# Performance work log

Measured on AMD Instinct MI355X. Metric: run time of the kernel, lower is better.

Reference implementation:

```python
import jax, jax.numpy as jnp
import numpy as np

S_IN = 14; KERNEL = 3; STRIDE = 1; C_IN = 32; C_OUT = 32; BATCH = 4; ROUTINGS = 3
EPS = 1e-7

def _child_parent_map(size_in, kernel, stride):
    # Same construction as BaseCaps._generate_voting_map: for each output position,
    # the flattened indices of its kernel window in the size_in x size_in grid.
    rows = []
    for row in range(0, size_in - kernel + 1, stride):
        for col in range(0, size_in - kernel + 1, stride):
            w = []
            for kr in range(kernel):
                start = (row + kr) * size_in + col
                w.extend(range(start, start + kernel))
            rows.append(w)
    return np.array(rows, dtype=np.int32)  # [size_out^2, kernel^2]

def setup_inputs() -> dict:
    key = jax.random.key(0)
    ks = jax.random.split(key, 5)
    in_act = jax.random.uniform(ks[0], (BATCH, S_IN, S_IN, C_IN, 1), jnp.float32)
    in_pose = jax.random.normal(ks[1], (BATCH, S_IN, S_IN, C_IN, 4, 4), jnp.float32)
    W = jax.random.normal(ks[2], (KERNEL * KERNEL * C_IN, C_OUT, 4, 4), jnp.float32) * 0.1
    beta_v = jax.random.normal(ks[3], (C_OUT,), jnp.float32)
    beta_a = jax.random.normal(ks[4], (C_OUT,), jnp.float32)
    cpm = jnp.asarray(_child_parent_map(S_IN, KERNEL, STRIDE))
    return {"in_act": in_act, "in_pose": in_pose, "transformation_weights": W,
            "beta_a": beta_a, "beta_v": beta_v, "child_parent_map": cpm}

def em_routing(act, votes, beta_a, beta_v, routings):
    # act: [B,P,K,1,1]  votes: [B,P,K,C,16]
    B, P, K, C, D = votes.shape
    rr = jnp.full((B, P, K, C, 1), 1.0 / C, votes.dtype)
    it_min, it_max = 1.0, max(1.0, min(float(routings), 3.0))
    out_a = out_mu = None
    for i in range(routings):
        inv_temp = it_min + (it_max - it_min) * (i / max(1.0, routings - 1.0))
        # --- M-step ---
        rp = rr * act                                        # [B,P,K,C,1]
        rs = rp.sum(axis=2, keepdims=True) + EPS             # [B,P,1,C,1]
        mu = (rp * votes).sum(axis=2, keepdims=True) / rs    # [B,P,1,C,D]
        var = (rp * (votes - mu) ** 2).sum(axis=2, keepdims=True) / rs + EPS
        cost = (beta_v[:, None] + 0.5 * jnp.log(var)) * rs   # [B,P,1,C,D]
        out_a = jax.nn.sigmoid(inv_temp * (beta_a[:, None] - cost.sum(-1, keepdims=True)))
        # --- E-step ---
        if i < routings - 1:
            log_p = -0.5 * jnp.sum(jnp.log(2.0 * jnp.pi * var) + (votes - mu) ** 2 / var,
                                   axis=-1, keepdims=True)   # [B,P,K,C,1]
            rr = jax.nn.softmax(jnp.log(out_a + EPS) + log_p, axis=3)
        out_mu = mu
    return out_a[:, :, 0, :, 0], out_mu[:, :, 0]  # [B,P,C], [B,P,C,D]

def reference(in_act, in_pose, transformation_weights, beta_a, beta_v, child_parent_map):
    B, S, _, Cin, _ = in_act.shape
    P, Kw = child_parent_map.shape           # [out_spatial^2, kernel^2]
    Sout = int(round(P ** 0.5))
    C = transformation_weights.shape[1]
    act = in_act.reshape(B, S * S, Cin)
    pose = in_pose.reshape(B, S * S, Cin, 4, 4)
    # gather kernel windows of child capsules per output position
    act_g = act[:, child_parent_map].reshape(B, P, Kw * Cin)             # [B,P,K]
    pose_g = pose[:, child_parent_map].reshape(B, P, Kw * Cin, 4, 4)     # [B,P,K,4,4]
    # votes = child_pose @ W, per (child k, parent capsule c)
    votes = jnp.einsum('bpkij,kcjl->bpkcil', pose_g, transformation_weights)
    votes = votes.reshape(B, P, Kw * Cin, C, 16)
    out_a, out_mu = em_routing(act_g[..., None, None], votes, beta_a, beta_v, ROUTINGS)
    out_act = out_a.reshape(B, Sout, Sout, C, 1)
    out_pose = out_mu.reshape(B, Sout, Sout, C, 4, 4)
    return out_act, out_pose
```

## Files before the change

kernel.cpp:

```cpp
#include <hip/hip_runtime.h>
#include <math.h>

#define NB 4
#define NP 144
#define KW 9
#define CIN 32
#define NC 32
#define NK 288
#define ND 16
#define NDH 8
#define EPSI 1e-7f
#define NT 256
#define KPT 36
#define NRED 2


typedef float v2f __attribute__((ext_vector_type(2)));

__device__ __forceinline__ v2f mkv2(float a, float b) { v2f r; r[0] = a; r[1] = b; return r; }

template<int CTRL>
__device__ __forceinline__ float dppf(float x) {
    return __int_as_float(__builtin_amdgcn_update_dpp(
        0, __float_as_int(x), CTRL, 0xF, 0xF, true));
}
__device__ __forceinline__ float swz16(float x) {
    return __int_as_float(__builtin_amdgcn_ds_swizzle(__float_as_int(x), 0x401F));
}
__device__ __forceinline__ float red16_max(float x) {
    x = fmaxf(x, dppf<0xB1>(x));
    x = fmaxf(x, dppf<0x4E>(x));
    x = fmaxf(x, dppf<0x141>(x));
    x = fmaxf(x, dppf<0x140>(x));
    return x;
}
__device__ __forceinline__ float red16_sum(float x) {
    x += dppf<0xB1>(x);
    x += dppf<0x4E>(x);
    x += dppf<0x141>(x);
    x += dppf<0x140>(x);
    return x;
}

__device__ __forceinline__ int sw4(int c, int j) { return j ^ ((c >> 1) & 3); }

__device__ __forceinline__ void load16(const float* src, float* dst) {
    const float4* s4 = (const float4*)src;
    *(float4*)&dst[0]  = s4[0];
    *(float4*)&dst[4]  = s4[1];
    *(float4*)&dst[8]  = s4[2];
    *(float4*)&dst[12] = s4[3];
}
__device__ __forceinline__ void load16v(const float* src, v2f* dst) {
    const float4* s4 = (const float4*)src;
    #pragma unroll
    for (int q = 0; q < 4; ++q) {
        const float4 tq = s4[q];
        dst[q*2+0] = mkv2(tq.x, tq.y);
        dst[q*2+1] = mkv2(tq.z, tq.w);
    }
}

__device__ __forceinline__ void vote44v(const float* pr, const v2f* wr2, v2f* v2) {
    #pragma unroll
    for (int i = 0; i < 4; ++i) {
        const v2f p0 = mkv2(pr[i*4+0], pr[i*4+0]);
        const v2f p1 = mkv2(pr[i*4+1], pr[i*4+1]);
        const v2f p2 = mkv2(pr[i*4+2], pr[i*4+2]);
        const v2f p3 = mkv2(pr[i*4+3], pr[i*4+3]);
        #pragma unroll
        for (int p = 0; p < 2; ++p) {
            v2f acc = p0 * wr2[0*2+p];
            acc += p1 * wr2[1*2+p];
            acc += p2 * wr2[2*2+p];
            acc += p3 * wr2[3*2+p];
            v2[i*2+p] = acc;
        }
    }
}

__device__ __forceinline__ void reduce_finalize(
    float r0, v2f m1v[NDH], v2f m2v[NDH],
    int t, int c, int wave, int lane, float inv_temp, bool last,
    float rbeta_a, float rbeta_v,
    float (&s_m1)[NRED][NC][ND], float (&s_m2)[NRED][NC][ND], float (&s_r0)[NRED][NC],
    float (&s_mu)[NC][17], float (&s_ivar)[NC][17], float (&s_A)[NC])
{
    float m1[ND], m2[ND];
    #pragma unroll
    for (int e = 0; e < NDH; ++e) {
        m1[2*e] = m1v[e][0]; m1[2*e+1] = m1v[e][1];
        m2[2*e] = m2v[e][0]; m2[2*e+1] = m2v[e][1];
    }
    r0 += __shfl_xor(r0, 32);
    #pragma unroll
    for (int d = 0; d < ND; ++d) {
        m1[d] += __shfl_xor(m1[d], 32);
        m2[d] += __shfl_xor(m2[d], 32);
    }
    if (lane < 32 && wave >= NRED) {
        float4* d1 = (float4*)&s_m1[wave - NRED][c][0];
        float4* d2 = (float4*)&s_m2[wave - NRED][c][0];
        #pragma unroll
        for (int j = 0; j < 4; ++j) {
            d1[sw4(c, j)] = *(const float4*)&m1[4*j];
            d2[sw4(c, j)] = *(const float4*)&m2[4*j];
        }
        s_r0[wave - NRED][c] = r0;
    }
    __syncthreads();
    if (lane < 32 && wave < NRED) {
        float4* d1 = (float4*)&s_m1[wave][c][0];
        float4* d2 = (float4*)&s_m2[wave][c][0];
        #pragma unroll
        for (int j = 0; j < 4; ++j) {
            float4 v1 = d1[sw4(c, j)];
            v1.x += m1[4*j]; v1.y += m1[4*j+1]; v1.z += m1[4*j+2]; v1.w += m1[4*j+3];
            d1[sw4(c, j)] = v1;
            float4 v2 = d2[sw4(c, j)];
            v2.x += m2[4*j]; v2.y += m2[4*j+1]; v2.z += m2[4*j+2]; v2.w += m2[4*j+3];
            d2[sw4(c, j)] = v2;
        }
        s_r0[wave][c] += r0;
    }
    __syncthreads();

    #pragma unroll
    for (int m = 0; m < 2; ++m) {
        const int item = t + m * NT;
        const int cc = item >> 4;
        const int d  = item & 15;
        const int fi = cc * ND + sw4(cc, d >> 2) * 4 + (d & 3);
        const float am1 = (&s_m1[0][0][0])[fi] + (&s_m1[1][0][0])[fi];
        const float am2 = (&s_m2[0][0][0])[fi] + (&s_m2[1][0][0])[fi];
        const float ar0 = s_r0[0][cc] + s_r0[1][cc];
        const float rs  = ar0 + EPSI;
        const float irs = __builtin_amdgcn_rcpf(rs);
        const float mu  = am1 * irs;
        const float var = (am2 - mu * (2.0f * am1 - mu * ar0)) * irs + EPSI;
        const float lv  = __logf(var);
        s_mu[cc][d]   = mu;
        s_ivar[cc][d] = __builtin_amdgcn_rcpf(var);
        const float Ls = red16_sum(lv);
        if (d == 0) s_A[cc] = Ls;
    }
    __syncthreads();

    if (t < NC) {
        const float log2pi16 = 16.0f * 1.8378770664093453f;
        const float ar0 = s_r0[0][t] + s_r0[1][t];
        const float rs = ar0 + EPSI;
        const float L  = s_A[t];
        const float costsum = rs * (16.0f * rbeta_v + 0.5f * L);
        const float x  = inv_temp * (rbeta_a - costsum);
        const float oa = 1.0f / (1.0f + __expf(-x));
        s_A[t] = last ? oa : (__logf(oa + EPSI) - 0.5f * (log2pi16 + L));
    }
    __syncthreads();
}

__global__ __launch_bounds__(NT) void convcaps_em_kernel(
    const float* __restrict__ g_act,
    const float* __restrict__ g_pose,
    const float* __restrict__ g_W,
    const float* __restrict__ g_beta_a,
    const float* __restrict__ g_beta_v,
    const int*   __restrict__ g_cpm,
    float* __restrict__ g_out)
{
    __shared__ float s_pose[NK][ND];
    __shared__ float s_act[NK];
    __shared__ float s_m1[NRED][NC][ND];
    __shared__ float s_m2[NRED][NC][ND];
    __shared__ float s_r0[NRED][NC];
    __shared__ float s_mu[NC][17];
    __shared__ float s_ivar[NC][17];
    __shared__ float s_A[NC];

    const int bp   = blockIdx.x;
    const int b    = bp / NP;
    const int p    = bp - b * NP;
    const int t    = threadIdx.x;
    const int c    = t & 31;
    const int s    = t >> 5;
    const int wave = t >> 6;
    const int lane = t & 63;

    float rbeta_a = 0.0f, rbeta_v = 0.0f;
    if (t < NC) { rbeta_a = g_beta_a[t]; rbeta_v = g_beta_v[t]; }

    {
        const int* cpm = g_cpm + p * KW;
        const float4* pb4 = (const float4*)(g_pose + (size_t)b * (196 * CIN * ND));
        float4* sp4 = (float4*)&s_pose[0][0];
        #pragma unroll 1
        for (int i4 = t; i4 < NK * ND / 4; i4 += NT) {
            const int w   = i4 >> 7;
            const int rem = i4 & 127;
            sp4[i4] = pb4[(size_t)cpm[w] * 128 + rem];
        }
        #pragma unroll 1
        for (int e = t; e < NK; e += NT)
            s_act[e] = g_act[(size_t)b * (196 * CIN) + cpm[e >> 5] * CIN + (e & 31)];
    }
    __syncthreads();

    const int    k0  = s * KPT;
    const float* wp0 = g_W + (size_t)(k0 * NC + c) * ND;

    {
        float r0 = 0.0f;
        v2f m1v[NDH], m2v[NDH];
        #pragma unroll
        for (int d = 0; d < NDH; ++d) { m1v[d] = mkv2(0,0); m2v[d] = mkv2(0,0); }

        const float* wp = wp0;
        #pragma unroll 1
        for (int jj = 0; jj < KPT; jj += 2, wp += 2 * NC * ND) {
            float pr[ND]; v2f wr[NDH];
            v2f va[NDH], vb[NDH];
            load16(&s_pose[k0 + jj][0], pr);
            load16v(wp, wr);
            vote44v(pr, wr, va);
            load16(&s_pose[k0 + jj + 1][0], pr);
            load16v(wp + NC * ND, wr);
            vote44v(pr, wr, vb);

            const float2 a2 = *(const float2*)&s_act[k0 + jj];
            const float rpa = a2.x * (1.0f / 32.0f);
            const float rpb = a2.y * (1.0f / 32.0f);
            r0 += rpa + rpb;
            const v2f rpav = mkv2(rpa, rpa), rpbv = mkv2(rpb, rpb);
            #pragma unroll
            for (int d = 0; d < NDH; ++d) {
                const v2f rva = rpav * va[d];
                const v2f rvb = rpbv * vb[d];
                m1v[d] += rva + rvb;
                m2v[d] += rva * va[d] + rvb * vb[d];
            }
        }
        reduce_finalize(r0, m1v, m2v, t, c, wave, lane, 1.0f, false, rbeta_a, rbeta_v,
                        s_m1, s_m2, s_r0, s_mu, s_ivar, s_A);
    }

    #pragma unroll 1
    for (int it = 1; it < 3; ++it) {
        const float L2E = 1.4426950408889634f;
        v2f iv2v[NDH], h2n2v[NDH];
        float gq2 = 0.0f;
        #pragma unroll
        for (int e = 0; e < NDH; ++e) {
            float ivs[2], hns[2];
            #pragma unroll
            for (int u = 0; u < 2; ++u) {
                const float mu  = s_mu[c][2*e+u];
                const float iv2 = s_ivar[c][2*e+u] * (0.5f * L2E);
                ivs[u] = iv2;
                const float h = iv2 * mu;
                hns[u] = -(h + h);
                gq2 = fmaf(h, mu, gq2);
            }
            iv2v[e]  = mkv2(ivs[0], ivs[1]);
            h2n2v[e] = mkv2(hns[0], hns[1]);
        }
        const float A2 = fmaf(L2E, s_A[c], -gq2);

        float r0 = 0.0f;
        v2f m1v[NDH], m2v[NDH];
        #pragma unroll
        for (int d = 0; d < NDH; ++d) { m1v[d] = mkv2(0,0); m2v[d] = mkv2(0,0); }

        const float* wp = wp0;
        #pragma unroll 1
        for (int jj = 0; jj < KPT; jj += 2, wp += 2 * NC * ND) {
            float pr[ND]; v2f wr[NDH];
            v2f va[NDH], vb[NDH];
            load16(&s_pose[k0 + jj][0], pr);
            load16v(wp, wr);
            vote44v(pr, wr, va);
            load16(&s_pose[k0 + jj + 1][0], pr);
            load16v(wp + NC * ND, wr);
            vote44v(pr, wr, vb);

            v2f qa2 = mkv2(0,0), qb2 = mkv2(0,0);
            #pragma unroll
            for (int e = 0; e < NDH; ++e) {
                qa2 += (iv2v[e] * va[e] + h2n2v[e]) * va[e];
                qb2 += (iv2v[e] * vb[e] + h2n2v[e]) * vb[e];
            }
            const float la = A2 - (qa2[0] + qa2[1]);
            const float lb = A2 - (qb2[0] + qb2[1]);

            const float ma = red16_max(la);
            const float mb = red16_max(lb);
            const float ea = __builtin_amdgcn_exp2f(la - ma);
            const float eb = __builtin_amdgcn_exp2f(lb - mb);
            const float sa = red16_sum(ea);
            const float sb = red16_sum(eb);
            const float mao = swz16(ma);
            const float sao = swz16(sa);
            const float mbo = swz16(mb);
            const float sbo = swz16(sb);
            const float Ma = fmaxf(ma, mao);
            const float Mb = fmaxf(mb, mbo);
            const float wa = __builtin_amdgcn_exp2f(ma - Ma);
            const float wb = __builtin_amdgcn_exp2f(mb - Mb);
            const float Sa = fmaf(sao, __builtin_amdgcn_exp2f(mao - Ma), sa * wa);
            const float Sb = fmaf(sbo, __builtin_amdgcn_exp2f(mbo - Mb), sb * wb);

            const float2 a2 = *(const float2*)&s_act[k0 + jj];
            const float rpa = ea * wa * __builtin_amdgcn_rcpf(Sa) * a2.x;
            const float rpb = eb * wb * __builtin_amdgcn_rcpf(Sb) * a2.y;
            r0 += rpa + rpb;
            const v2f rpav = mkv2(rpa, rpa), rpbv = mkv2(rpb, rpb);
            #pragma unroll
            for (int d = 0; d < NDH; ++d) {
                const v2f rva = rpav * va[d];
                const v2f rvb = rpbv * vb[d];
                m1v[d] += rva + rvb;
                m2v[d] += rva * va[d] + rvb * vb[d];
            }
        }
        reduce_finalize(r0, m1v, m2v, t, c, wave, lane, 1.0f + (float)it, it == 2,
                        rbeta_a, rbeta_v,
                        s_m1, s_m2, s_r0, s_mu, s_ivar, s_A);
    }

    const int base = (b * NP + p) * NC;
    if (t < NC) g_out[base + t] = s_A[t];
    float* outpose = g_out + NB * NP * NC;
    #pragma unroll
    for (int m = 0; m < 2; ++m) {
        const int item = t + m * NT;
        const int cc = item >> 4;
        const int d  = item & 15;
        outpose[(size_t)(base + cc) * ND + d] = s_mu[cc][d];
    }
}

extern "C" void kernel_launch(void* const* d_in, const int* in_sizes, int n_in,
                              void* d_out, int out_size, void* d_ws, size_t ws_size,
                              hipStream_t stream) {
    const float* in_act  = (const float*)d_in[0];
    const float* in_pose = (const float*)d_in[1];
    const float* W       = (const float*)d_in[2];
    const float* beta_a  = (const float*)d_in[3];
    const float* beta_v  = (const float*)d_in[4];
    const int*   cpm     = (const int*)d_in[5];
    float* out = (float*)d_out;

    convcaps_em_kernel<<<dim3(NB * NP), dim3(NT), 0, stream>>>(
        in_act, in_pose, W, beta_a, beta_v, cpm, out);
}
```

Before: 97.73 us.

## Remap lanes so softmax over capsules uses permlane32 swap, not swizzle merge

Changes the thread-to-(capsule, k-slice) mapping so each wave's 32 capsules for one child sit in lanes 0-15 and 32-47 (and likewise for the second slice). The softmax across capsules then reduces with DPP within 16 lanes plus a permlane32 swap, or a shfl_xor fallback, instead of two-half online-softmax merging with extra exps and swizzles. The final cross-slice reduction switches from shfl_xor 32 to swizzle. This trims per-iteration ALU and exp work in the hot E-step loop, but the weight loads are now less contiguous across lanes.

```diff
diff --git a/kernel.cpp b/kernel.cpp
--- a/kernel.cpp
+++ b/kernel.cpp
@@ -9,6 +9,7 @@
 #define NK 288
 #define ND 16
 #define NDH 8
+#define NCND 512
 #define EPSI 1e-7f
 #define NT 256
 #define KPT 36
@@ -16,6 +17,7 @@
 
 
 typedef float v2f __attribute__((ext_vector_type(2)));
+typedef int   v2i __attribute__((ext_vector_type(2)));
 
 __device__ __forceinline__ v2f mkv2(float a, float b) { v2f r; r[0] = a; r[1] = b; return r; }
 
@@ -27,12 +29,34 @@
 __device__ __forceinline__ float swz16(float x) {
     return __int_as_float(__builtin_amdgcn_ds_swizzle(__float_as_int(x), 0x401F));
 }
-__device__ __forceinline__ float red16_max(float x) {
+
+#if __has_builtin(__builtin_amdgcn_permlane32_swap)
+__device__ __forceinline__ float xmax32(float x) {
+    v2i r = __builtin_amdgcn_permlane32_swap(__float_as_int(x), __float_as_int(x), false, false);
+    return fmaxf(__int_as_float(r[0]), __int_as_float(r[1]));
+}
+__device__ __forceinline__ float xsum32(float x) {
+    v2i r = __builtin_amdgcn_permlane32_swap(__float_as_int(x), __float_as_int(x), false, false);
+    return __int_as_float(r[0]) + __int_as_float(r[1]);
+}
+#else
+__device__ __forceinline__ float xmax32(float x) { return fmaxf(x, __shfl_xor(x, 32)); }
+__device__ __forceinline__ float xsum32(float x) { return x + __shfl_xor(x, 32); }
+#endif
+
+__device__ __forceinline__ float red32c_max(float x) {
     x = fmaxf(x, dppf<0xB1>(x));
     x = fmaxf(x, dppf<0x4E>(x));
     x = fmaxf(x, dppf<0x141>(x));
     x = fmaxf(x, dppf<0x140>(x));
-    return x;
+    return xmax32(x);
+}
+__device__ __forceinline__ float red32c_sum(float x) {
+    x += dppf<0xB1>(x);
+    x += dppf<0x4E>(x);
+    x += dppf<0x141>(x);
+    x += dppf<0x140>(x);
+    return xsum32(x);
 }
 __device__ __forceinline__ float red16_sum(float x) {
     x += dppf<0xB1>(x);
@@ -61,7 +85,7 @@
     }
 }
 
-__device__ __forceinline__ void vote44v(const float* pr, const v2f* wr2, v2f* v2) {
+__device__ __forceinline__ void vote44v(const float* pr, const v2f* wr2, v2f* v) {
     #pragma unroll
     for (int i = 0; i < 4; ++i) {
         const v2f p0 = mkv2(pr[i*4+0], pr[i*4+0]);
@@ -74,7 +98,7 @@
             acc += p1 * wr2[1*2+p];
             acc += p2 * wr2[2*2+p];
             acc += p3 * wr2[3*2+p];
-            v2[i*2+p] = acc;
+            v[i*2+p] = acc;
         }
     }
 }
@@ -92,13 +116,14 @@
         m1[2*e] = m1v[e][0]; m1[2*e+1] = m1v[e][1];
         m2[2*e] = m2v[e][0]; m2[2*e+1] = m2v[e][1];
     }
-    r0 += __shfl_xor(r0, 32);
+    r0 += swz16(r0);
     #pragma unroll
     for (int d = 0; d < ND; ++d) {
-        m1[d] += __shfl_xor(m1[d], 32);
-        m2[d] += __shfl_xor(m2[d], 32);
-    }
-    if (lane < 32 && wave >= NRED) {
+        m1[d] += swz16(m1[d]);
+        m2[d] += swz16(m2[d]);
+    }
+    const bool wlane = (lane & 16) == 0;
+    if (wlane && wave >= NRED) {
         float4* d1 = (float4*)&s_m1[wave - NRED][c][0];
         float4* d2 = (float4*)&s_m2[wave - NRED][c][0];
         #pragma unroll
@@ -109,7 +134,7 @@
         s_r0[wave - NRED][c] = r0;
     }
     __syncthreads();
-    if (lane < 32 && wave < NRED) {
+    if (wlane && wave < NRED) {
         float4* d1 = (float4*)&s_m1[wave][c][0];
         float4* d2 = (float4*)&s_m2[wave][c][0];
         #pragma unroll
@@ -181,10 +206,11 @@
     const int b    = bp / NP;
     const int p    = bp - b * NP;
     const int t    = threadIdx.x;
-    const int c    = t & 31;
-    const int s    = t >> 5;
+    const int lane = t & 63;
     const int wave = t >> 6;
-    const int lane = t & 63;
+    const int c    = (lane & 15) | ((lane >> 1) & 16);
+    const int kpar = (lane >> 4) & 1;
+    const int sl   = wave * 2 + kpar;
 
     float rbeta_a = 0.0f, rbeta_v = 0.0f;
     if (t < NC) { rbeta_a = g_beta_a[t]; rbeta_v = g_beta_v[t]; }
@@ -205,7 +231,7 @@
     }
     __syncthreads();
 
-    const int    k0  = s * KPT;
+    const int    k0  = sl * KPT;
     const float* wp0 = g_W + (size_t)(k0 * NC + c) * ND;
 
     {
@@ -216,14 +242,14 @@
 
         const float* wp = wp0;
         #pragma unroll 1
-        for (int jj = 0; jj < KPT; jj += 2, wp += 2 * NC * ND) {
+        for (int jj = 0; jj < KPT; jj += 2, wp += 2 * NCND) {
             float pr[ND]; v2f wr[NDH];
             v2f va[NDH], vb[NDH];
             load16(&s_pose[k0 + jj][0], pr);
             load16v(wp, wr);
             vote44v(pr, wr, va);
             load16(&s_pose[k0 + jj + 1][0], pr);
-            load16v(wp + NC * ND, wr);
+            load16v(wp + NCND, wr);
             vote44v(pr, wr, vb);
 
             const float2 a2 = *(const float2*)&s_act[k0 + jj];
@@ -272,14 +298,14 @@
 
         const float* wp = wp0;
         #pragma unroll 1
-        for (int jj = 0; jj < KPT; jj += 2, wp += 2 * NC * ND) {
+        for (int jj = 0; jj < KPT; jj += 2, wp += 2 * NCND) {
             float pr[ND]; v2f wr[NDH];
             v2f va[NDH], vb[NDH];
             load16(&s_pose[k0 + jj][0], pr);
             load16v(wp, wr);
             vote44v(pr, wr, va);
             load16(&s_pose[k0 + jj + 1][0], pr);
-            load16v(wp + NC * ND, wr);
+            load16v(wp + NCND, wr);
             vote44v(pr, wr, vb);
 
             v2f qa2 = mkv2(0,0), qb2 = mkv2(0,0);
@@ -291,26 +317,16 @@
             const float la = A2 - (qa2[0] + qa2[1]);
             const float lb = A2 - (qb2[0] + qb2[1]);
 
-            const float ma = red16_max(la);
-            const float mb = red16_max(lb);
+            const float ma = red32c_max(la);
+            const float mb = red32c_max(lb);
             const float ea = __builtin_amdgcn_exp2f(la - ma);
             const float eb = __builtin_amdgcn_exp2f(lb - mb);
-            const float sa = red16_sum(ea);
-            const float sb = red16_sum(eb);
-            const float mao = swz16(ma);
-            const float sao = swz16(sa);
-            const float mbo = swz16(mb);
-            const float sbo = swz16(sb);
-            const float Ma = fmaxf(ma, mao);
-            const float Mb = fmaxf(mb, mbo);
-            const float wa = __builtin_amdgcn_exp2f(ma - Ma);
-            const float wb = __builtin_amdgcn_exp2f(mb - Mb);
-            const float Sa = fmaf(sao, __builtin_amdgcn_exp2f(mao - Ma), sa * wa);
-            const float Sb = fmaf(sbo, __builtin_amdgcn_exp2f(mbo - Mb), sb * wb);
+            const float sa = red32c_sum(ea);
+            const float sb = red32c_sum(eb);
 
             const float2 a2 = *(const float2*)&s_act[k0 + jj];
-            const float rpa = ea * wa * __builtin_amdgcn_rcpf(Sa) * a2.x;
-            const float rpb = eb * wb * __builtin_amdgcn_rcpf(Sb) * a2.y;
+            const float rpa = ea * __builtin_amdgcn_rcpf(sa) * a2.x;
+            const float rpb = eb * __builtin_amdgcn_rcpf(sb) * a2.y;
             r0 += rpa + rpb;
             const v2f rpav = mkv2(rpa, rpa), rpbv = mkv2(rpb, rpb);
             #pragma unroll
```

After: 109.6 us. 1.12x slower.

## Split EM routing into per-iteration pass and combine kernels over halved K

Applied to the files above, without the earlier changes.

Replaces the single fused kernel with six launches: three pass kernels, each splitting the 288 child capsules into two halves per (batch, position), and three combine kernels that merge partial moments into mu, inverse variance and activation. Partials and stats go through workspace memory. This doubles the block count to fill more compute units. The cost is extra launches and global round trips for the partial sums and routing stats. The old fused kernel stays as a fallback when the workspace is too small.

```diff
diff --git a/kernel.cpp b/kernel.cpp
--- a/kernel.cpp
+++ b/kernel.cpp
@@ -3,17 +3,28 @@
 
 #define NB 4
 #define NP 144
+#define NBP (NB*NP)
 #define KW 9
 #define CIN 32
 #define NC 32
 #define NK 288
 #define ND 16
 #define NDH 8
+#define NCND 512
 #define EPSI 1e-7f
+
+#define NTS 192
+#define KH  144
+#define KPTS 24
+#define NGR 3
+#define PART_F 1056
+#define STATS_F 1056
+#define WS_PART_FLOATS ((size_t)2*NBP*PART_F)
+#define WS_NEEDED ((WS_PART_FLOATS + (size_t)NBP*STATS_F) * 4)
+
 #define NT 256
 #define KPT 36
 #define NRED 2
-
 
 typedef float v2f __attribute__((ext_vector_type(2)));
 
@@ -61,7 +72,7 @@
     }
 }
 
-__device__ __forceinline__ void vote44v(const float* pr, const v2f* wr2, v2f* v2) {
+__device__ __forceinline__ void vote44v(const float* pr, const v2f* wr2, v2f* v) {
     #pragma unroll
     for (int i = 0; i < 4; ++i) {
         const v2f p0 = mkv2(pr[i*4+0], pr[i*4+0]);
@@ -74,12 +85,248 @@
             acc += p1 * wr2[1*2+p];
             acc += p2 * wr2[2*2+p];
             acc += p3 * wr2[3*2+p];
-            v2[i*2+p] = acc;
-        }
-    }
-}
-
-__device__ __forceinline__ void reduce_finalize(
+            v[i*2+p] = acc;
+        }
+    }
+}
+
+template<bool FIRST>
+__global__ __launch_bounds__(NTS) void convcaps_pass(
+    const float* __restrict__ g_act,
+    const float* __restrict__ g_pose,
+    const float* __restrict__ g_W,
+    const int*   __restrict__ g_cpm,
+    const float* __restrict__ g_stats,
+    float* __restrict__ g_part)
+{
+    __shared__ float s_pose[KH][ND];
+    __shared__ float s_act[KH];
+    __shared__ float s_m1[NGR][NC][ND];
+    __shared__ float s_m2[NGR][NC][ND];
+    __shared__ float s_r0[NGR][NC];
+
+    const int bid  = blockIdx.x;
+    const int g    = bid / NBP;
+    const int bp   = bid - g * NBP;
+    const int b    = bp / NP;
+    const int p    = bp - b * NP;
+    const int t    = threadIdx.x;
+    const int c    = t & 31;
+    const int sl   = t >> 5;
+    const int wave = t >> 6;
+    const int lane = t & 63;
+
+    {
+        const int* cpm = g_cpm + p * KW;
+        const float4* pb4 = (const float4*)(g_pose + (size_t)b * (196 * CIN * ND));
+        float4* sp4 = (float4*)&s_pose[0][0];
+        #pragma unroll 1
+        for (int i4 = t; i4 < KH * 4; i4 += NTS) {
+            const int kk  = g * KH + (i4 >> 2);
+            const int w   = kk >> 5;
+            const int rem = ((kk & 31) << 2) | (i4 & 3);
+            sp4[i4] = pb4[(size_t)cpm[w] * 128 + rem];
+        }
+        const float* ab = g_act + (size_t)b * (196 * CIN);
+        if (t < KH) {
+            const int kk = g * KH + t;
+            s_act[t] = ab[cpm[kk >> 5] * CIN + (kk & 31)];
+        }
+    }
+
+    const float L2E = 1.4426950408889634f;
+    v2f iv2v[NDH], h2n2v[NDH];
+    float A2 = 0.0f;
+    if (!FIRST) {
+        const float* st = g_stats + (size_t)bp * STATS_F;
+        float gq2 = 0.0f;
+        #pragma unroll
+        for (int e = 0; e < NDH; ++e) {
+            float ivs[2], hns[2];
+            #pragma unroll
+            for (int u = 0; u < 2; ++u) {
+                const float mu  = st[c * ND + 2*e + u];
+                const float iv2 = st[NCND + c * ND + 2*e + u] * (0.5f * L2E);
+                ivs[u] = iv2;
+                const float h = iv2 * mu;
+                hns[u] = -(h + h);
+                gq2 = fmaf(h, mu, gq2);
+            }
+            iv2v[e]  = mkv2(ivs[0], ivs[1]);
+            h2n2v[e] = mkv2(hns[0], hns[1]);
+        }
+        A2 = fmaf(L2E, st[2 * NCND + c], -gq2);
+    }
+    __syncthreads();
+
+    const int    k0  = sl * KPTS;
+    const float* wp0 = g_W + (size_t)((g * KH + k0) * NC + c) * ND;
+
+    float r0 = 0.0f;
+    v2f m1v[NDH], m2v[NDH];
+    #pragma unroll
+    for (int d = 0; d < NDH; ++d) { m1v[d] = mkv2(0,0); m2v[d] = mkv2(0,0); }
+
+    const float* wp = wp0;
+    #pragma unroll 1
+    for (int jj = 0; jj < KPTS; jj += 2, wp += 2 * NCND) {
+        float pr[ND]; v2f wr[NDH];
+        v2f va[NDH], vb[NDH];
+        load16(&s_pose[k0 + jj][0], pr);
+        load16v(wp, wr);
+        vote44v(pr, wr, va);
+        load16(&s_pose[k0 + jj + 1][0], pr);
+        load16v(wp + NCND, wr);
+        vote44v(pr, wr, vb);
+
+        const float2 a2 = *(const float2*)&s_act[k0 + jj];
+        float rpa, rpb;
+        if (FIRST) {
+            rpa = a2.x * (1.0f / 32.0f);
+            rpb = a2.y * (1.0f / 32.0f);
+        } else {
+            v2f qa2 = mkv2(0,0), qb2 = mkv2(0,0);
+            #pragma unroll
+            for (int e = 0; e < NDH; ++e) {
+                qa2 += (iv2v[e] * va[e] + h2n2v[e]) * va[e];
+                qb2 += (iv2v[e] * vb[e] + h2n2v[e]) * vb[e];
+            }
+            const float la = A2 - (qa2[0] + qa2[1]);
+            const float lb = A2 - (qb2[0] + qb2[1]);
+
+            const float ma = red16_max(la);
+            const float mb = red16_max(lb);
+            const float ea = __builtin_amdgcn_exp2f(la - ma);
+            const float eb = __builtin_amdgcn_exp2f(lb - mb);
+            const float sa = red16_sum(ea);
+            const float sb = red16_sum(eb);
+            const float mao = swz16(ma);
+            const float sao = swz16(sa);
+            const float mbo = swz16(mb);
+            const float sbo = swz16(sb);
+            const float Ma = fmaxf(ma, mao);
+            const float Mb = fmaxf(mb, mbo);
+            const float wa = __builtin_amdgcn_exp2f(ma - Ma);
+            const float wb = __builtin_amdgcn_exp2f(mb - Mb);
+            const float Sa = fmaf(sao, __builtin_amdgcn_exp2f(mao - Ma), sa * wa);
+            const float Sb = fmaf(sbo, __builtin_amdgcn_exp2f(mbo - Mb), sb * wb);
+            rpa = ea * wa * __builtin_amdgcn_rcpf(Sa) * a2.x;
+            rpb = eb * wb * __builtin_amdgcn_rcpf(Sb) * a2.y;
+        }
+
+        r0 += rpa + rpb;
+        const v2f rpav = mkv2(rpa, rpa), rpbv = mkv2(rpb, rpb);
+        #pragma unroll
+        for (int d = 0; d < NDH; ++d) {
+            const v2f rva = rpav * va[d];
+            const v2f rvb = rpbv * vb[d];
+            m1v[d] += rva + rvb;
+            m2v[d] += rva * va[d] + rvb * vb[d];
+        }
+    }
+
+    float m1[ND], m2[ND];
+    #pragma unroll
+    for (int e = 0; e < NDH; ++e) {
+        m1[2*e] = m1v[e][0]; m1[2*e+1] = m1v[e][1];
+        m2[2*e] = m2v[e][0]; m2[2*e+1] = m2v[e][1];
+    }
+    r0 += __shfl_xor(r0, 32);
+    #pragma unroll
+    for (int d = 0; d < ND; ++d) {
+        m1[d] += __shfl_xor(m1[d], 32);
+        m2[d] += __shfl_xor(m2[d], 32);
+    }
+    if (lane < 32) {
+        float4* d1 = (float4*)&s_m1[wave][c][0];
+        float4* d2 = (float4*)&s_m2[wave][c][0];
+        #pragma unroll
+        for (int j = 0; j < 4; ++j) {
+            d1[sw4(c, j)] = *(const float4*)&m1[4*j];
+            d2[sw4(c, j)] = *(const float4*)&m2[4*j];
+        }
+        s_r0[wave][c] = r0;
+    }
+    __syncthreads();
+
+    float* my_part = g_part + (size_t)bid * PART_F;
+    #pragma unroll 1
+    for (int i = t; i < PART_F; i += NTS) {
+        float v;
+        if (i < NCND) {
+            const int cc = i >> 4, d = i & 15;
+            const int fi = cc*ND + sw4(cc, d>>2)*4 + (d&3);
+            v = (&s_m1[0][0][0])[fi] + (&s_m1[1][0][0])[fi] + (&s_m1[2][0][0])[fi];
+        } else if (i < 2*NCND) {
+            const int j = i - NCND;
+            const int cc = j >> 4, d = j & 15;
+            const int fi = cc*ND + sw4(cc, d>>2)*4 + (d&3);
+            v = (&s_m2[0][0][0])[fi] + (&s_m2[1][0][0])[fi] + (&s_m2[2][0][0])[fi];
+        } else {
+            const int cc = i - 2*NCND;
+            v = s_r0[0][cc] + s_r0[1][cc] + s_r0[2][cc];
+        }
+        my_part[i] = v;
+    }
+}
+
+__global__ __launch_bounds__(512) void convcaps_combine(
+    const float* __restrict__ g_part,
+    float* __restrict__ g_stats,
+    const float* __restrict__ g_beta_a,
+    const float* __restrict__ g_beta_v,
+    float* __restrict__ g_out,
+    float inv_temp, int last)
+{
+    __shared__ float sL[NC];
+    const int bp = blockIdx.x;
+    const int t  = threadIdx.x;
+    const int cc = t >> 4;
+    const int d  = t & 15;
+
+    const float* p0 = g_part + (size_t)bp * PART_F;
+    const float* p1 = g_part + (size_t)(bp + NBP) * PART_F;
+
+    const float am1 = p0[t] + p1[t];
+    const float am2 = p0[NCND + t] + p1[NCND + t];
+    const float ar0 = p0[2*NCND + cc] + p1[2*NCND + cc];
+    const float rs  = ar0 + EPSI;
+    const float irs = __builtin_amdgcn_rcpf(rs);
+    const float mu  = am1 * irs;
+    const float var = (am2 - mu * (2.0f * am1 - mu * ar0)) * irs + EPSI;
+    const float lv  = __logf(var);
+    const float Ls  = red16_sum(lv);
+    if (d == 0) sL[cc] = Ls;
+
+    if (!last) {
+        float* st = g_stats + (size_t)bp * STATS_F;
+        st[t]        = mu;
+        st[NCND + t] = __builtin_amdgcn_rcpf(var);
+    } else {
+        float* outpose = g_out + NBP * NC;
+        outpose[(size_t)(bp * NC + cc) * ND + d] = mu;
+    }
+    __syncthreads();
+
+    if (t < NC) {
+        const float log2pi16 = 16.0f * 1.8378770664093453f;
+        const float ar0c = p0[2*NCND + t] + p1[2*NCND + t];
+        const float rsc  = ar0c + EPSI;
+        const float L    = sL[t];
+        const float costsum = rsc * (16.0f * g_beta_v[t] + 0.5f * L);
+        const float x  = inv_temp * (g_beta_a[t] - costsum);
+        const float oa = 1.0f / (1.0f + __expf(-x));
+        if (!last) {
+            float* st = g_stats + (size_t)bp * STATS_F;
+            st[2*NCND + t] = __logf(oa + EPSI) - 0.5f * (log2pi16 + L);
+        } else {
+            g_out[bp * NC + t] = oa;
+        }
+    }
+}
+
+
+__device__ __forceinline__ void reduce_finalize_fb(
     float r0, v2f m1v[NDH], v2f m2v[NDH],
     int t, int c, int wave, int lane, float inv_temp, bool last,
     float rbeta_a, float rbeta_v,
@@ -216,14 +463,14 @@
 
         const float* wp = wp0;
         #pragma unroll 1
-        for (int jj = 0; jj < KPT; jj += 2, wp += 2 * NC * ND) {
+        for (int jj = 0; jj < KPT; jj += 2, wp += 2 * NCND) {
             float pr[ND]; v2f wr[NDH];
             v2f va[NDH], vb[NDH];
             load16(&s_pose[k0 + jj][0], pr);
             load16v(wp, wr);
             vote44v(pr, wr, va);
             load16(&s_pose[k0 + jj + 1][0], pr);
-            load16v(wp + NC * ND, wr);
+            load16v(wp + NCND, wr);
             vote44v(pr, wr, vb);
 
             const float2 a2 = *(const float2*)&s_act[k0 + jj];
@@ -239,8 +486,8 @@
                 m2v[d] += rva * va[d] + rvb * vb[d];
             }
         }
-        reduce_finalize(r0, m1v, m2v, t, c, wave, lane, 1.0f, false, rbeta_a, rbeta_v,
-                        s_m1, s_m2, s_r0, s_mu, s_ivar, s_A);
+        reduce_finalize_fb(r0, m1v, m2v, t, c, wave, lane, 1.0f, false, rbeta_a, rbeta_v,
+                           s_m1, s_m2, s_r0, s_mu, s_ivar, s_A);
     }
 
     #pragma unroll 1
@@ -272,14 +519,14 @@
 
         const float* wp = wp0;
         #pragma unroll 1
-        for (int jj = 0; jj < KPT; jj += 2, wp += 2 * NC * ND) {
+        for (int jj = 0; jj < KPT; jj += 2, wp += 2 * NCND) {
             float pr[ND]; v2f wr[NDH];
             v2f va[NDH], vb[NDH];
             load16(&s_pose[k0 + jj][0], pr);
             load16v(wp, wr);
             vote44v(pr, wr, va);
             load16(&s_pose[k0 + jj + 1][0], pr);
-            load16v(wp + NC * ND, wr);
+            load16v(wp + NCND, wr);
             vote44v(pr, wr, vb);
 
             v2f qa2 = mkv2(0,0), qb2 = mkv2(0,0);
@@ -321,14 +568,14 @@
                 m2v[d] += rva * va[d] + rvb * vb[d];
             }
         }
-        reduce_finalize(r0, m1v, m2v, t, c, wave, lane, 1.0f + (float)it, it == 2,
-                        rbeta_a, rbeta_v,
-                        s_m1, s_m2, s_r0, s_mu, s_ivar, s_A);
-    }
-
-    const int base = (b * NP + p) * NC;
+        reduce_finalize_fb(r0, m1v, m2v, t, c, wave, lane, 1.0f + (float)it, it == 2,
+                           rbeta_a, rbeta_v,
+                           s_m1, s_m2, s_r0, s_mu, s_ivar, s_A);
+    }
+
+    const int base = bp * NC;
     if (t < NC) g_out[base + t] = s_A[t];
-    float* outpose = g_out + NB * NP * NC;
+    float* outpose = g_out + NBP * NC;
     #pragma unroll
     for (int m = 0; m < 2; ++m) {
         const int item = t + m * NT;
@@ -349,6 +596,23 @@
     const int*   cpm     = (const int*)d_in[5];
     float* out = (float*)d_out;
 
-    convcaps_em_kernel<<<dim3(NB * NP), dim3(NT), 0, stream>>>(
-        in_act, in_pose, W, beta_a, beta_v, cpm, out);
-}
+    if (ws_size >= WS_NEEDED && d_ws != nullptr) {
+        float* part  = (float*)d_ws;
+        float* stats = part + WS_PART_FLOATS;
+        convcaps_pass<true><<<dim3(2 * NBP), dim3(NTS), 0, stream>>>(
+            in_act, in_pose, W, cpm, stats, part);
+        convcaps_combine<<<dim3(NBP), dim3(512), 0, stream>>>(
+            part, stats, beta_a, beta_v, out, 1.0f, 0);
+        convcaps_pass<false><<<dim3(2 * NBP), dim3(NTS), 0, stream>>>(
+            in_act, in_pose, W, cpm, stats, part);
+        convcaps_combine<<<dim3(NBP), dim3(512), 0, stream>>>(
+            part, stats, beta_a, beta_v, out, 2.0f, 0);
+        convcaps_pass<false><<<dim3(2 * NBP), dim3(NTS), 0, stream>>>(
+            in_act, in_pose, W, cpm, stats, part);
+        convcaps_combine<<<dim3(NBP), dim3(512), 0, stream>>>(
+            part, stats, beta_a, beta_v, out, 3.0f, 1);
+    } else {
+        convcaps_em_kernel<<<dim3(NBP), dim3(NT), 0, stream>>>(
+            in_act, in_pose, W, beta_a, beta_v, cpm, out);
+    }
+}
```

New measurement: 115.1 us. 1.18x slower.
